# Optimization experiments

Hardware: AMD Instinct MI355X
Metric: run time of the kernel (lower is better)

Reference implementation:

```python
import jax, jax.numpy as jnp
import numpy as np

B, N1, N2, H, LAT, MID = 16, 2048, 2048, 768, 128, 256


def setup_inputs() -> dict:
    key = jax.random.key(0)
    ks = jax.random.split(key, 20)
    def lin(k, n_in, n_out):
        s = 1.0 / np.sqrt(n_in)
        kw, kb = jax.random.split(k)
        W = jax.random.uniform(kw, (n_in, n_out), jnp.float32, -s, s)
        b = jax.random.uniform(kb, (n_out,), jnp.float32, -s, s)
        return W, b
    We1, be1 = lin(ks[0], H, MID)
    We2, be2 = lin(ks[1], MID, LAT)
    Wq, bq = lin(ks[2], LAT, LAT)
    Wk, bk = lin(ks[3], LAT, LAT)
    Wv, bv = lin(ks[4], LAT, LAT)
    Wd1, bd1 = lin(ks[5], LAT, MID)
    Wd2, bd2 = lin(ks[6], MID, H)
    main_feature = jax.random.normal(ks[7], (B, N1, H), jnp.float32)
    feature = jax.random.normal(ks[8], (B, N2, H), jnp.float32)
    return dict(main_feature=main_feature, feature=feature,
                We1=We1, be1=be1, We2=We2, be2=be2,
                Wq=Wq, bq=bq, Wk=Wk, bk=bk, Wv=Wv, bv=bv,
                Wd1=Wd1, bd1=bd1, Wd2=Wd2, bd2=bd2)


def reference(main_feature, feature, We1, be1, We2, be2, Wq, bq, Wk, bk, Wv, bv, Wd1, bd1, Wd2, bd2):
    def encode(x):
        h = jax.nn.relu(x @ We1 + be1)
        return jax.nn.relu(h @ We2 + be2)  # [B, N, LAT]

    def decode(x):
        h = jax.nn.relu(x @ Wd1 + bd1)
        return jax.nn.sigmoid(h @ Wd2 + bd2)  # [B, N, H]

    m = encode(main_feature)           # [B, N1, LAT]
    f = encode(feature)                # [B, N2, LAT]
    q = m @ Wq + bq                    # [B, N1, LAT]
    k = f @ Wk + bk                    # [B, N2, LAT]
    v = f @ Wv + bv                    # [B, N2, LAT]
    scores = jnp.einsum('bnd,bmd->bnm', q, k)   # unscaled, [B, N1, N2]
    probs = jax.nn.softmax(scores, axis=-1)
    attn = jnp.einsum('bnm,bmd->bnd', probs, v)  # [B, N1, LAT]
    return decode(attn)                # [B, N1, H]
```

## Files before the change

kernel.cpp:

```cpp
#include <hip/hip_runtime.h>
#include <stdint.h>

typedef unsigned short u16;
typedef __bf16 bf16x8 __attribute__((ext_vector_type(8)));
typedef float f32x4 __attribute__((ext_vector_type(4)));

#define MM   32768

#define WAITV(N) asm volatile("s_waitcnt vmcnt(" #N ")" ::: "memory")
#define WAITL0() asm volatile("s_waitcnt lgkmcnt(0)" ::: "memory")
#define BARR()   do { asm volatile("" ::: "memory"); __builtin_amdgcn_s_barrier(); \
                      asm volatile("" ::: "memory"); } while (0)

__device__ __forceinline__ u16 f2bf(float f) {
    uint32_t u; __builtin_memcpy(&u, &f, 4);
    u += 0x7fffu + ((u >> 16) & 1u);
    return (u16)(u >> 16);
}

__device__ __forceinline__ void gl_lds16(const u16* g, u16* l) {
    __builtin_amdgcn_global_load_lds(
        (__attribute__((address_space(1))) void*)(g),
        (__attribute__((address_space(3))) void*)(l), 16, 0, 0);
}

__global__ void transpose_all(const float* __restrict__ We1, const float* __restrict__ We2,
                              const float* __restrict__ Wq,  const float* __restrict__ Wk,
                              const float* __restrict__ Wv,  const float* __restrict__ Wd1,
                              const float* __restrict__ Wd2, u16* __restrict__ wt) {
    int i = blockIdx.x * 256 + threadIdx.x;
    const float* src; int K, N, off;
    if      (i < 196608) { src = We1; K = 768; N = 256; off = i;          }
    else if (i < 229376) { src = We2; K = 256; N = 128; off = i - 196608; }
    else if (i < 245760) { src = Wq;  K = 128; N = 128; off = i - 229376; }
    else if (i < 262144) { src = Wk;  K = 128; N = 128; off = i - 245760; }
    else if (i < 278528) { src = Wv;  K = 128; N = 128; off = i - 262144; }
    else if (i < 311296) { src = Wd1; K = 128; N = 256; off = i - 278528; }
    else if (i < 507904) { src = Wd2; K = 256; N = 768; off = i - 311296; }
    else return;
    int n = off / K, k = off % K;
    wt[i] = f2bf(src[(size_t)k * N + n]);
}

template <int BM, int ACT, bool TRANS, bool A_F32, bool OUT_F32>
__global__ void gemm_bt(const void* __restrict__ Avp, const u16* __restrict__ Wt,
                        const float* __restrict__ bias, void* __restrict__ Cvp,
                        int M, int N, int K) {
    constexpr int MI  = BM / 32;
    constexpr int AF4 = BM / 16;
    __shared__ u16 a_sh[2][BM * 64];
    __shared__ u16 b_sh[2][128 * 64];
    const int t = threadIdx.x;
    const int wave = t >> 6, lane = t & 63;
    const int lrow = lane & 15, quad = lane >> 4;
    const int wr = wave >> 1, wc = wave & 1;
    const int m0 = blockIdx.x * BM, n0 = blockIdx.y * 128;

    const float* Af = (const float*)Avp;
    const u16*   Ab = (const u16*)Avp;

    f32x4 acc[MI][4];
#pragma unroll
    for (int i = 0; i < MI; i++)
#pragma unroll
        for (int j = 0; j < 4; j++) acc[i][j] = (f32x4){0.f, 0.f, 0.f, 0.f};

    float4 pf[A_F32 ? AF4 : 1];

    auto stage_b = [&](int buf, int k0) {
#pragma unroll
        for (int it = 0; it < 4; it++) {
            int s = it * 256 + t;
            gl_lds16(Wt + (size_t)(n0 + (s >> 3)) * K + k0 + (s & 7) * 8,
                     &b_sh[buf][(it * 256 + wave * 64) * 8]);
        }
    };
    auto stage_a_bf = [&](int buf, int k0) {
#pragma unroll
        for (int it = 0; it < BM / 32; it++) {
            int s = it * 256 + t;
            gl_lds16(Ab + (size_t)(m0 + (s >> 3)) * K + k0 + (s & 7) * 8,
                     &a_sh[buf][(it * 256 + wave * 64) * 8]);
        }
    };
    auto load_a_f32 = [&](int k0) {
#pragma unroll
        for (int it = 0; it < AF4; it++) {
            int s = it * 256 + t;
            pf[it] = *(const float4*)(Af + (size_t)(m0 + (s >> 4)) * K + k0 + (s & 15) * 4);
        }
    };
    auto write_a_f32 = [&](int buf) {
#pragma unroll
        for (int it = 0; it < AF4; it++) {
            int s = it * 256 + t;
            int row = s >> 4, kc = s & 15;
            float4 v = pf[it];
            uint32_t p0 = (uint32_t)f2bf(v.x) | ((uint32_t)f2bf(v.y) << 16);
            uint32_t p1 = (uint32_t)f2bf(v.z) | ((uint32_t)f2bf(v.w) << 16);
            *(uint32_t*)&a_sh[buf][row * 64 + kc * 4]     = p0;
            *(uint32_t*)&a_sh[buf][row * 64 + kc * 4 + 2] = p1;
        }
    };
    auto compute = [&](int buf) {
#pragma unroll
        for (int kk = 0; kk < 2; kk++) {
            bf16x8 af[MI], bfv[4];
#pragma unroll
            for (int i = 0; i < MI; i++)
                af[i] = *(const bf16x8*)&a_sh[buf][(wr * (BM / 2) + i * 16 + lrow) * 64 + kk * 32 + quad * 8];
#pragma unroll
            for (int j = 0; j < 4; j++)
                bfv[j] = *(const bf16x8*)&b_sh[buf][(wc * 64 + j * 16 + lrow) * 64 + kk * 32 + quad * 8];
            __builtin_amdgcn_s_setprio(1);
#pragma unroll
            for (int i = 0; i < MI; i++)
#pragma unroll
                for (int j = 0; j < 4; j++)
                    acc[i][j] = __builtin_amdgcn_mfma_f32_16x16x32_bf16(af[i], bfv[j], acc[i][j], 0, 0, 0);
            __builtin_amdgcn_s_setprio(0);
        }
    };

    const int T = K >> 6;
    if (A_F32) {
        load_a_f32(0); stage_b(0, 0);
        WAITV(4);
        write_a_f32(0);
        WAITL0(); WAITV(0);
    } else {
        stage_a_bf(0, 0); stage_b(0, 0);
        WAITV(0);
    }
    BARR();

    int cur = 0;
    for (int tt = 0; tt < T; ++tt) {
        const int nk = (tt + 1) * 64;
        const bool more = nk < K;
        if (more) {
            if (A_F32) load_a_f32(nk); else stage_a_bf(cur ^ 1, nk);
            stage_b(cur ^ 1, nk);
        }
        if (tt > 0) {
            if (more) { if (A_F32) { WAITV(8); } else { WAITV(6); } }
            else      { WAITV(0); }
            BARR();
        }
        compute(cur);
        if (A_F32 && more) {
            WAITV(4);
            write_a_f32(cur ^ 1);
            WAITL0();
        }
        if (more) BARR();
        cur ^= 1;
    }

    float bv4[4];
#pragma unroll
    for (int j = 0; j < 4; j++) bv4[j] = bias[n0 + wc * 64 + j * 16 + lrow];

#pragma unroll
    for (int i = 0; i < MI; i++) {
#pragma unroll
        for (int j = 0; j < 4; j++) {
            const int col = n0 + wc * 64 + j * 16 + lrow;
            if (!TRANS) {
#pragma unroll
                for (int r = 0; r < 4; r++) {
                    float x = acc[i][j][r] + bv4[j];
                    if (ACT == 1) x = fmaxf(x, 0.f);
                    if (ACT == 2) x = 1.f / (1.f + __expf(-x));
                    const int row = m0 + wr * (BM / 2) + i * 16 + quad * 4 + r;
                    if (OUT_F32) ((float*)Cvp)[(size_t)row * N + col] = x;
                    else         ((u16*)Cvp)[(size_t)row * N + col] = f2bf(x);
                }
            } else {
                u16 vv[4];
#pragma unroll
                for (int r = 0; r < 4; r++) vv[r] = f2bf(acc[i][j][r] + bv4[j]);
                u16* Cb = (u16*)Cvp;
                size_t base = (size_t)(m0 >> 11) * ((size_t)N * 2048) + (size_t)col * 2048 +
                              (m0 & 2047) + wr * (BM / 2) + i * 16 + quad * 4;
                *(uint32_t*)&Cb[base]     = (uint32_t)vv[0] | ((uint32_t)vv[1] << 16);
                *(uint32_t*)&Cb[base + 2] = (uint32_t)vv[2] | ((uint32_t)vv[3] << 16);
            }
        }
    }
}

__global__ __launch_bounds__(256)
void flash_attn(const u16* __restrict__ Q, const u16* __restrict__ Kb,
                const u16* __restrict__ VT, u16* __restrict__ O) {
    __shared__ u16 kb_sh[2][64 * 128];
    __shared__ u16 v_sh[128 * 64];
    __shared__ u16 qp_sh[64 * 128];

    const int t = threadIdx.x, wave = t >> 6, lane = t & 63;
    const int lrow = lane & 15, quad = lane >> 4;
    const int lsw = (lrow & 7) << 3;
    const int b = blockIdx.x >> 5, q0 = (blockIdx.x & 31) * 64;

    int ksrc[4], vsrc[4], ldst[4];
#pragma unroll
    for (int it = 0; it < 4; it++) {
        int s = it * 256 + t;
        ksrc[it] = (s ^ ((s >> 4) & 7)) * 8;
        int row = s >> 3, cc = (s & 7) ^ (row & 7);
        vsrc[it] = row * 2048 + cc * 8;
        ldst[it] = (it * 256 + wave * 64) * 8;
    }

    const u16* qg  = Q  + (size_t)(b * 2048 + q0) * 128;
    const u16* kgb = Kb + (size_t)b * 2048 * 128;
    const u16* vgb = VT + (size_t)b * 262144;

#pragma unroll
    for (int it = 0; it < 4; it++) gl_lds16(qg + ksrc[it], &qp_sh[ldst[it]]);
#pragma unroll
    for (int it = 0; it < 4; it++) gl_lds16(kgb + ksrc[it], &kb_sh[0][ldst[it]]);
#pragma unroll
    for (int it = 0; it < 4; it++) gl_lds16(vgb + vsrc[it], &v_sh[ldst[it]]);
    WAITV(8); BARR();
    bf16x8 qf[4];
#pragma unroll
    for (int ks = 0; ks < 4; ks++)
        qf[ks] = *(const bf16x8*)&qp_sh[(((wave * 16 + lrow) * 128) + ks * 32 + quad * 8) ^ lsw];

    f32x4 o_acc[8];
#pragma unroll
    for (int ct = 0; ct < 8; ct++) o_acc[ct] = (f32x4){0.f, 0.f, 0.f, 0.f};
    float m_i[4] = {-1e30f, -1e30f, -1e30f, -1e30f};
    float l_i[4] = {0.f, 0.f, 0.f, 0.f};

    for (int tile = 0; tile < 32; tile++) {
        const int c = tile & 1;
        const u16* kg_n = kgb + (size_t)(((tile + 1) & 31) * 64) * 128;
#pragma unroll
        for (int it = 0; it < 4; it++) gl_lds16(kg_n + ksrc[it], &kb_sh[c ^ 1][ldst[it]]);
        WAITV(8); BARR();

        f32x4 s_acc[4];
        __builtin_amdgcn_s_setprio(1);
#pragma unroll
        for (int ct = 0; ct < 4; ct++) {
            f32x4 a = (f32x4){0.f, 0.f, 0.f, 0.f};
#pragma unroll
            for (int ks = 0; ks < 4; ks++) {
                bf16x8 kf = *(const bf16x8*)&kb_sh[c][(((ct * 16 + lrow) * 128) + ks * 32 + quad * 8) ^ lsw];
                a = __builtin_amdgcn_mfma_f32_16x16x32_bf16(qf[ks], kf, a, 0, 0, 0);
            }
            s_acc[ct] = a;
        }
        __builtin_amdgcn_s_setprio(0);

        float mnew[4], alpha[4], ps[4];
#pragma unroll
        for (int r = 0; r < 4; r++) {
            float mx = s_acc[0][r];
#pragma unroll
            for (int ct = 1; ct < 4; ct++) mx = fmaxf(mx, s_acc[ct][r]);
#pragma unroll
            for (int d = 8; d >= 1; d >>= 1) mx = fmaxf(mx, __shfl_xor(mx, d, 64));
            mnew[r] = fmaxf(m_i[r], mx);
            alpha[r] = __expf(m_i[r] - mnew[r]);
            m_i[r] = mnew[r];
            ps[r] = 0.f;
        }
#pragma unroll
        for (int ct = 0; ct < 4; ct++)
#pragma unroll
            for (int r = 0; r < 4; r++) {
                float p = __expf(s_acc[ct][r] - mnew[r]);
                ps[r] += p;
                qp_sh[(((wave * 16 + quad * 4 + r) * 128) + ct * 16 + lrow) ^ (((quad * 4 + r) & 7) << 3)] = f2bf(p);
            }
#pragma unroll
        for (int r = 0; r < 4; r++) {
#pragma unroll
            for (int d = 8; d >= 1; d >>= 1) ps[r] += __shfl_xor(ps[r], d, 64);
            l_i[r] = l_i[r] * alpha[r] + ps[r];
        }
#pragma unroll
        for (int ct = 0; ct < 8; ct++)
#pragma unroll
            for (int r = 0; r < 4; r++) o_acc[ct][r] *= alpha[r];

        WAITV(4); BARR();

        bf16x8 pfa[2];
#pragma unroll
        for (int ks = 0; ks < 2; ks++)
            pfa[ks] = *(const bf16x8*)&qp_sh[(((wave * 16 + lrow) * 128) + ks * 32 + quad * 8) ^ lsw];
        __builtin_amdgcn_s_setprio(1);
#pragma unroll
        for (int ct = 0; ct < 8; ct++)
#pragma unroll
            for (int ks = 0; ks < 2; ks++) {
                bf16x8 vf = *(const bf16x8*)&v_sh[(((ct * 16 + lrow) * 64) + ks * 32 + quad * 8) ^ lsw];
                o_acc[ct] = __builtin_amdgcn_mfma_f32_16x16x32_bf16(pfa[ks], vf, o_acc[ct], 0, 0, 0);
            }
        __builtin_amdgcn_s_setprio(0);

        if (tile < 31) {
            BARR();
            const u16* vg_n = vgb + (tile + 1) * 64;
#pragma unroll
            for (int it = 0; it < 4; it++) gl_lds16(vg_n + vsrc[it], &v_sh[ldst[it]]);
        }
    }

    float inv_l[4];
#pragma unroll
    for (int r = 0; r < 4; r++) inv_l[r] = 1.f / l_i[r];
#pragma unroll
    for (int ct = 0; ct < 8; ct++)
#pragma unroll
        for (int r = 0; r < 4; r++) {
            const int row = b * 2048 + q0 + wave * 16 + quad * 4 + r;
            O[(size_t)row * 128 + ct * 16 + lrow] = f2bf(o_acc[ct][r] * inv_l[r]);
        }
}

extern "C" void kernel_launch(void* const* d_in, const int* in_sizes, int n_in,
                              void* d_out, int out_size, void* d_ws, size_t ws_size,
                              hipStream_t stream) {
    const float* mainf = (const float*)d_in[0];
    const float* feat  = (const float*)d_in[1];
    const float* We1 = (const float*)d_in[2];  const float* be1 = (const float*)d_in[3];
    const float* We2 = (const float*)d_in[4];  const float* be2 = (const float*)d_in[5];
    const float* Wq  = (const float*)d_in[6];  const float* bq  = (const float*)d_in[7];
    const float* Wk  = (const float*)d_in[8];  const float* bk  = (const float*)d_in[9];
    const float* Wv  = (const float*)d_in[10]; const float* bv  = (const float*)d_in[11];
    const float* Wd1 = (const float*)d_in[12]; const float* bd1 = (const float*)d_in[13];
    const float* Wd2 = (const float*)d_in[14]; const float* bd2 = (const float*)d_in[15];

    u16* ws = (u16*)d_ws;
    u16* wt = ws;
    u16* h1 = wt + 524288;
    u16* mf = h1 + 8388608;
    u16* qb = mf + 4194304;
    u16* kb = qb + 4194304;
    u16* vT = kb + 4194304;
    u16* wt_e1 = wt, *wt_e2 = wt + 196608, *wt_q = wt + 229376, *wt_k = wt + 245760,
       * wt_v = wt + 262144, *wt_d1 = wt + 278528, *wt_d2 = wt + 311296;

    transpose_all<<<1984, 256, 0, stream>>>(We1, We2, Wq, Wk, Wv, Wd1, Wd2, wt);

    gemm_bt<64, 1, false, true,  false><<<dim3(512, 2), 256, 0, stream>>>(mainf, wt_e1, be1, h1, MM, 256, 768);
    gemm_bt<64, 1, false, false, false><<<dim3(512, 1), 256, 0, stream>>>(h1,    wt_e2, be2, mf, MM, 128, 256);
    gemm_bt<64, 0, false, false, false><<<dim3(512, 1), 256, 0, stream>>>(mf,    wt_q,  bq,  qb, MM, 128, 128);
    gemm_bt<64, 1, false, true,  false><<<dim3(512, 2), 256, 0, stream>>>(feat, wt_e1, be1, h1, MM, 256, 768);
    gemm_bt<64, 1, false, false, false><<<dim3(512, 1), 256, 0, stream>>>(h1,   wt_e2, be2, mf, MM, 128, 256);
    gemm_bt<64, 0, false, false, false><<<dim3(512, 1), 256, 0, stream>>>(mf,   wt_k,  bk,  kb, MM, 128, 128);
    gemm_bt<64, 0, true,  false, false><<<dim3(512, 1), 256, 0, stream>>>(mf,   wt_v,  bv,  vT, MM, 128, 128);

    flash_attn<<<512, 256, 0, stream>>>(qb, kb, vT, mf);

    gemm_bt<64, 1, false, false, false><<<dim3(512, 2), 256, 0, stream>>>(mf, wt_d1, bd1, h1, MM, 256, 128);
    gemm_bt<64, 2, false, false, true ><<<dim3(512, 6), 256, 0, stream>>>(h1, wt_d2, bd2, d_out, MM, 768, 256);
}
```

Measured before the change: 498.5 us.

## Add weight-resident small GEMM kernel and simplify flash attention tile loading

Adds a gemm_small kernel that keeps the whole weight matrix in LDS and gives each wave one 16-row strip. It is used for the narrow-N projections (We2, Wq, Wk, Wv, Wd1) to cut per-block staging overhead and raise parallelism per block. The flash attention kernel also drops its double-buffered K prefetch and split V load. It now loads K and V synchronously at the start of each tile with full __syncthreads barriers, which removes the overlap of global loads with compute. The A fragments in gemm_small are read directly from global memory with strided 16-byte loads.

```diff
diff --git a/kernel.cpp b/kernel.cpp
--- a/kernel.cpp
+++ b/kernel.cpp
@@ -42,6 +42,66 @@
     wt[i] = f2bf(src[(size_t)k * N + n]);
 }
 
+template <int N, int K, int ACT, bool TRANS>
+__global__ __launch_bounds__(512)
+void gemm_small(const u16* __restrict__ A, const u16* __restrict__ Wt,
+                const float* __restrict__ bias, u16* __restrict__ C) {
+    __shared__ u16 w_sh[N * K];
+    const int t = threadIdx.x, wave = t >> 6, lane = t & 63;
+    const int lrow = lane & 15, quad = lane >> 4;
+    constexpr int SEGS = N * K / 8;
+
+    for (int s = t; s < SEGS; s += 512) {
+        int n = s / (K / 8), kc = s % (K / 8);
+        bf16x8 w = *(const bf16x8*)&Wt[(size_t)n * K + kc * 8];
+        *(bf16x8*)&w_sh[(n * K + kc * 8) ^ ((n & 7) << 3)] = w;
+    }
+    float bv[N / 16];
+#pragma unroll
+    for (int j = 0; j < N / 16; j++) bv[j] = bias[j * 16 + lrow];
+    __syncthreads();
+
+    const int strip = blockIdx.x * 8 + wave;
+    const int row0 = strip * 16;
+
+    bf16x8 af[K / 32];
+#pragma unroll
+    for (int ks = 0; ks < K / 32; ks++)
+        af[ks] = *(const bf16x8*)&A[(size_t)(row0 + lrow) * K + ks * 32 + quad * 8];
+
+    f32x4 acc[N / 16];
+#pragma unroll
+    for (int j = 0; j < N / 16; j++) acc[j] = (f32x4){0.f, 0.f, 0.f, 0.f};
+#pragma unroll
+    for (int j = 0; j < N / 16; j++)
+#pragma unroll
+        for (int ks = 0; ks < K / 32; ks++) {
+            bf16x8 wf = *(const bf16x8*)&w_sh[((j * 16 + lrow) * K + ks * 32 + quad * 8) ^ ((lrow & 7) << 3)];
+            acc[j] = __builtin_amdgcn_mfma_f32_16x16x32_bf16(af[ks], wf, acc[j], 0, 0, 0);
+        }
+
+#pragma unroll
+    for (int j = 0; j < N / 16; j++) {
+        const int col = j * 16 + lrow;
+        if (!TRANS) {
+#pragma unroll
+            for (int r = 0; r < 4; r++) {
+                float x = acc[j][r] + bv[j];
+                if (ACT == 1) x = fmaxf(x, 0.f);
+                C[(size_t)(row0 + quad * 4 + r) * N + col] = f2bf(x);
+            }
+        } else {
+            u16 vv[4];
+#pragma unroll
+            for (int r = 0; r < 4; r++) vv[r] = f2bf(acc[j][r] + bv[j]);
+            size_t base = (size_t)(row0 >> 11) * ((size_t)N * 2048) + (size_t)col * 2048 +
+                          (row0 & 2047) + quad * 4;
+            *(uint32_t*)&C[base]     = (uint32_t)vv[0] | ((uint32_t)vv[1] << 16);
+            *(uint32_t*)&C[base + 2] = (uint32_t)vv[2] | ((uint32_t)vv[3] << 16);
+        }
+    }
+}
+
 template <int BM, int ACT, bool TRANS, bool A_F32, bool OUT_F32>
 __global__ void gemm_bt(const void* __restrict__ Avp, const u16* __restrict__ Wt,
                         const float* __restrict__ bias, void* __restrict__ Cvp,
@@ -193,7 +253,7 @@
 __global__ __launch_bounds__(256)
 void flash_attn(const u16* __restrict__ Q, const u16* __restrict__ Kb,
                 const u16* __restrict__ VT, u16* __restrict__ O) {
-    __shared__ u16 kb_sh[2][64 * 128];
+    __shared__ u16 k_sh[64 * 128];
     __shared__ u16 v_sh[128 * 64];
     __shared__ u16 qp_sh[64 * 128];
 
@@ -202,27 +262,14 @@
     const int lsw = (lrow & 7) << 3;
     const int b = blockIdx.x >> 5, q0 = (blockIdx.x & 31) * 64;
 
-    int ksrc[4], vsrc[4], ldst[4];
+    const u16* qg = Q + (size_t)(b * 2048 + q0) * 128;
 #pragma unroll
     for (int it = 0; it < 4; it++) {
         int s = it * 256 + t;
-        ksrc[it] = (s ^ ((s >> 4) & 7)) * 8;
-        int row = s >> 3, cc = (s & 7) ^ (row & 7);
-        vsrc[it] = row * 2048 + cc * 8;
-        ldst[it] = (it * 256 + wave * 64) * 8;
-    }
-
-    const u16* qg  = Q  + (size_t)(b * 2048 + q0) * 128;
-    const u16* kgb = Kb + (size_t)b * 2048 * 128;
-    const u16* vgb = VT + (size_t)b * 262144;
-
-#pragma unroll
-    for (int it = 0; it < 4; it++) gl_lds16(qg + ksrc[it], &qp_sh[ldst[it]]);
-#pragma unroll
-    for (int it = 0; it < 4; it++) gl_lds16(kgb + ksrc[it], &kb_sh[0][ldst[it]]);
-#pragma unroll
-    for (int it = 0; it < 4; it++) gl_lds16(vgb + vsrc[it], &v_sh[ldst[it]]);
-    WAITV(8); BARR();
+        int srcSeg = s ^ ((s >> 4) & 7);
+        gl_lds16(qg + (size_t)srcSeg * 8, &qp_sh[(it * 256 + wave * 64) * 8]);
+    }
+    __syncthreads();
     bf16x8 qf[4];
 #pragma unroll
     for (int ks = 0; ks < 4; ks++)
@@ -235,11 +282,22 @@
     float l_i[4] = {0.f, 0.f, 0.f, 0.f};
 
     for (int tile = 0; tile < 32; tile++) {
-        const int c = tile & 1;
-        const u16* kg_n = kgb + (size_t)(((tile + 1) & 31) * 64) * 128;
-#pragma unroll
-        for (int it = 0; it < 4; it++) gl_lds16(kg_n + ksrc[it], &kb_sh[c ^ 1][ldst[it]]);
-        WAITV(8); BARR();
+        const u16* kg = Kb + (size_t)(b * 2048 + tile * 64) * 128;
+        const u16* vg = VT + (size_t)b * 262144 + tile * 64;
+#pragma unroll
+        for (int it = 0; it < 4; it++) {
+            int s = it * 256 + t;
+            int srcSeg = s ^ ((s >> 4) & 7);
+            gl_lds16(kg + (size_t)srcSeg * 8, &k_sh[(it * 256 + wave * 64) * 8]);
+        }
+#pragma unroll
+        for (int it = 0; it < 4; it++) {
+            int s = it * 256 + t;
+            int row = s >> 3, c = (s & 7) ^ (row & 7);
+            gl_lds16(vg + (size_t)row * 2048 + c * 8,
+                     &v_sh[(it * 256 + wave * 64) * 8]);
+        }
+        __syncthreads();
 
         f32x4 s_acc[4];
         __builtin_amdgcn_s_setprio(1);
@@ -248,7 +306,7 @@
             f32x4 a = (f32x4){0.f, 0.f, 0.f, 0.f};
 #pragma unroll
             for (int ks = 0; ks < 4; ks++) {
-                bf16x8 kf = *(const bf16x8*)&kb_sh[c][(((ct * 16 + lrow) * 128) + ks * 32 + quad * 8) ^ lsw];
+                bf16x8 kf = *(const bf16x8*)&k_sh[(((ct * 16 + lrow) * 128) + ks * 32 + quad * 8) ^ lsw];
                 a = __builtin_amdgcn_mfma_f32_16x16x32_bf16(qf[ks], kf, a, 0, 0, 0);
             }
             s_acc[ct] = a;
@@ -287,8 +345,6 @@
 #pragma unroll
             for (int r = 0; r < 4; r++) o_acc[ct][r] *= alpha[r];
 
-        WAITV(4); BARR();
-
         bf16x8 pfa[2];
 #pragma unroll
         for (int ks = 0; ks < 2; ks++)
@@ -302,13 +358,7 @@
                 o_acc[ct] = __builtin_amdgcn_mfma_f32_16x16x32_bf16(pfa[ks], vf, o_acc[ct], 0, 0, 0);
             }
         __builtin_amdgcn_s_setprio(0);
-
-        if (tile < 31) {
-            BARR();
-            const u16* vg_n = vgb + (tile + 1) * 64;
-#pragma unroll
-            for (int it = 0; it < 4; it++) gl_lds16(vg_n + vsrc[it], &v_sh[ldst[it]]);
-        }
+        __syncthreads();
     }
 
     float inv_l[4];
@@ -349,15 +399,15 @@
     transpose_all<<<1984, 256, 0, stream>>>(We1, We2, Wq, Wk, Wv, Wd1, Wd2, wt);
 
     gemm_bt<64, 1, false, true,  false><<<dim3(512, 2), 256, 0, stream>>>(mainf, wt_e1, be1, h1, MM, 256, 768);
-    gemm_bt<64, 1, false, false, false><<<dim3(512, 1), 256, 0, stream>>>(h1,    wt_e2, be2, mf, MM, 128, 256);
-    gemm_bt<64, 0, false, false, false><<<dim3(512, 1), 256, 0, stream>>>(mf,    wt_q,  bq,  qb, MM, 128, 128);
+    gemm_small<128, 256, 1, false><<<256, 512, 0, stream>>>(h1, wt_e2, be2, mf);
+    gemm_small<128, 128, 0, false><<<256, 512, 0, stream>>>(mf, wt_q,  bq,  qb);
     gemm_bt<64, 1, false, true,  false><<<dim3(512, 2), 256, 0, stream>>>(feat, wt_e1, be1, h1, MM, 256, 768);
-    gemm_bt<64, 1, false, false, false><<<dim3(512, 1), 256, 0, stream>>>(h1,   wt_e2, be2, mf, MM, 128, 256);
-    gemm_bt<64, 0, false, false, false><<<dim3(512, 1), 256, 0, stream>>>(mf,   wt_k,  bk,  kb, MM, 128, 128);
-    gemm_bt<64, 0, true,  false, false><<<dim3(512, 1), 256, 0, stream>>>(mf,   wt_v,  bv,  vT, MM, 128, 128);
+    gemm_small<128, 256, 1, false><<<256, 512, 0, stream>>>(h1, wt_e2, be2, mf);
+    gemm_small<128, 128, 0, false><<<256, 512, 0, stream>>>(mf, wt_k,  bk,  kb);
+    gemm_small<128, 128, 0, true ><<<256, 512, 0, stream>>>(mf, wt_v,  bv,  vT);
 
     flash_attn<<<512, 256, 0, stream>>>(qb, kb, vT, mf);
 
-    gemm_bt<64, 1, false, false, false><<<dim3(512, 2), 256, 0, stream>>>(mf, wt_d1, bd1, h1, MM, 256, 128);
+    gemm_small<256, 128, 1, false><<<256, 512, 0, stream>>>(mf, wt_d1, bd1, h1);
     gemm_bt<64, 2, false, false, true ><<<dim3(512, 6), 256, 0, stream>>>(h1, wt_d2, bd2, d_out, MM, 768, 256);
 }
```

After: 492.2 us. Within noise of the previous version (-1.3%).
